# Kernel tuning notes

Hardware: AMD Instinct MI355X
Metric: run time of the kernel (lower is better)

The kernel has to match this reference:

```python
import jax, jax.numpy as jnp
import numpy as np

NUM_HEAD = 16
D = 1024
HEAD_DIM = D // NUM_HEAD
EPS = 1e-5


def setup_inputs() -> dict:
    key = jax.random.key(0)
    ks = jax.random.split(key, 7)
    B, S = 2, 2048
    s = 1.0 / np.sqrt(D)
    return {
        "x": jax.random.normal(ks[0], (B, S, D), dtype=jnp.float32),
        "wq": jax.random.uniform(ks[1], (D, D), jnp.float32, -s, s),
        "bq": jax.random.uniform(ks[2], (D,), jnp.float32, -s, s),
        "wk": jax.random.uniform(ks[3], (D, D), jnp.float32, -s, s),
        "bk": jax.random.uniform(ks[4], (D,), jnp.float32, -s, s),
        "wv": jax.random.uniform(ks[5], (D, D), jnp.float32, -s, s),
        "bv": jax.random.uniform(ks[6], (D,), jnp.float32, -s, s),
        "gamma": jnp.ones((D,), jnp.float32),
        "beta": jnp.zeros((D,), jnp.float32),
    }


def reference(x, wq, bq, wk, bk, wv, bv, gamma, beta):
    B, S, Dm = x.shape
    # Linear: x @ W^T + b (torch convention), then split heads -> [B, H, S, hd]
    def proj(w, b):
        y = jnp.einsum("bsd,ed->bse", x, w) + b
        return y.reshape(B, S, NUM_HEAD, HEAD_DIM).transpose(0, 2, 1, 3)

    q = proj(wq, bq)
    k = proj(wk, bk)
    v = proj(wv, bv)

    scores = jnp.einsum("bhqd,bhkd->bhqk", q, k) / np.sqrt(HEAD_DIM).astype(x.dtype)
    attn = jax.nn.softmax(scores, axis=-1)
    out = jnp.einsum("bhqk,bhkd->bhqd", attn, v)
    out = out.transpose(0, 2, 1, 3).reshape(B, S, Dm)

    out = out + x
    mu = jnp.mean(out, axis=-1, keepdims=True)
    var = jnp.var(out, axis=-1, keepdims=True)
    out = (out - mu) * jax.lax.rsqrt(var + EPS) * gamma + beta
    return out
```

## Files before the change

kernel.cpp:

```cpp
#include <hip/hip_runtime.h>

typedef unsigned short u16;
typedef unsigned int   u32;
typedef __bf16 bf16x8 __attribute__((ext_vector_type(8)));
typedef float  f32x4  __attribute__((ext_vector_type(4)));

#define D_MODEL 1024
#define SEQ     2048
#define NHEAD   16
#define HD      64
#define SOFTMAX_SCL 0.18033688011112042f

__device__ __forceinline__ u16 f2bf(float f) {
    u32 u;
    __builtin_memcpy(&u, &f, 4);
    u32 r = (u + 0x7fffu + ((u >> 16) & 1u)) >> 16;
    return (u16)r;
}
__device__ __forceinline__ float bf2f(u16 v) {
    u32 u = ((u32)v) << 16;
    float f;
    __builtin_memcpy(&f, &u, 4);
    return f;
}

__device__ __forceinline__ void async_copy16(const u16* g, u16* l) {
    __builtin_amdgcn_global_load_lds(
        (__attribute__((address_space(1))) void*)g,
        (__attribute__((address_space(3))) void*)l, 16, 0, 0);
}

__device__ __forceinline__ uint2 pack4(float a, float b, float c, float d) {
    uint2 r;
    r.x = (u32)f2bf(a) | ((u32)f2bf(b) << 16);
    r.y = (u32)f2bf(c) | ((u32)f2bf(d) << 16);
    return r;
}

#define NX4 ((2 * SEQ * D_MODEL) / 4)
#define NW4 ((D_MODEL * D_MODEL) / 4)
__global__ __launch_bounds__(256) void conv_all(
    const float* __restrict__ x,  const float* __restrict__ wq,
    const float* __restrict__ wk, const float* __restrict__ wv,
    u16* __restrict__ xb, u16* __restrict__ wqb,
    u16* __restrict__ wkb, u16* __restrict__ wvb)
{
    int i = blockIdx.x * 256 + threadIdx.x;
    const float* src; u16* dst; int off;
    if (i < NX4)            { src = x;  dst = xb;  off = i; }
    else if (i < NX4 + NW4) { src = wq; dst = wqb; off = i - NX4; }
    else if (i < NX4 + 2 * NW4) { src = wk; dst = wkb; off = i - NX4 - NW4; }
    else                    { src = wv; dst = wvb; off = i - NX4 - 2 * NW4; }
    float4 a = ((const float4*)src)[off];
    ushort4 o;
    o.x = f2bf(a.x); o.y = f2bf(a.y); o.z = f2bf(a.z); o.w = f2bf(a.w);
    ((ushort4*)dst)[off] = o;
}

__global__ __launch_bounds__(256) void qkv_gemm(
    const u16* __restrict__ xb,
    const u16* __restrict__ wqb, const float* __restrict__ bq,
    const u16* __restrict__ wkb, const float* __restrict__ bk,
    const u16* __restrict__ wvb, const float* __restrict__ bv,
    u16* __restrict__ qb, u16* __restrict__ kb, u16* __restrict__ vt)
{
    const int bid  = blockIdx.x;
    const int pair = bid % 24;
    const int by   = bid / 24;
    const int z    = pair >> 3;
    const int bx   = pair & 7;

    const u16* Ap; const u16* Bp;
    int m0, n0;
    if (z < 2) {
        Ap = (z == 1) ? wkb : wqb;  Bp = xb;
        m0 = bx * 128;
        n0 = by * 128;
    } else {
        Ap = xb;  Bp = wvb;
        m0 = by * 128;
        n0 = bx * 128;
    }

    __shared__ u16 As[128 * 64];
    __shared__ u16 Bs[128 * 64];

    const int tid  = threadIdx.x;
    const int wave = tid >> 6;
    const int lane = tid & 63;
    const int quad = lane >> 4;
    const int l16  = lane & 15;
    const int wm   = wave >> 1;
    const int wn   = wave & 1;
    const int swz  = l16 & 7;

    int rr[4], co[4];
#pragma unroll
    for (int t = 0; t < 4; ++t) {
        int ch = (wave * 4 + t) * 64 + lane;
        rr[t] = ch >> 3;
        co[t] = ((ch & 7) ^ (rr[t] & 7)) * 8;
    }

    f32x4 acc[4][4] = {};

    for (int kt = 0; kt < D_MODEL; kt += 64) {
        __syncthreads();
#pragma unroll
        for (int t = 0; t < 4; ++t) {
            int chbase = (wave * 4 + t) * 64;
            async_copy16(Ap + (size_t)(m0 + rr[t]) * D_MODEL + kt + co[t], As + chbase * 8);
            async_copy16(Bp + (size_t)(n0 + rr[t]) * D_MODEL + kt + co[t], Bs + chbase * 8);
        }
        __syncthreads();

#pragma unroll
        for (int kc = 0; kc < 2; ++kc) {
            bf16x8 af[4], bf_[4];
#pragma unroll
            for (int i = 0; i < 4; ++i)
                af[i] = *(const bf16x8*)&As[(wm * 64 + i * 16 + l16) * 64 + (((kc * 4 + quad) ^ swz) << 3)];
#pragma unroll
            for (int j = 0; j < 4; ++j)
                bf_[j] = *(const bf16x8*)&Bs[(wn * 64 + j * 16 + l16) * 64 + (((kc * 4 + quad) ^ swz) << 3)];
#pragma unroll
            for (int i = 0; i < 4; ++i)
#pragma unroll
                for (int j = 0; j < 4; ++j)
                    acc[i][j] = __builtin_amdgcn_mfma_f32_16x16x32_bf16(af[i], bf_[j], acc[i][j], 0, 0, 0);
        }
    }

    const int chunk_lo = (quad & 1) * 4;
    if (z < 2) {
        u16* out = (z == 1) ? kb : qb;
        const float* bi = (z == 1) ? bk : bq;
        const float scl = (z == 1) ? 1.0f : SOFTMAX_SCL;
        const int fblk = m0 + wm * 64;
#pragma unroll
        for (int i = 0; i < 4; ++i) {
            const int fb = fblk + i * 16 + quad * 4;
            float4 b4 = *(const float4*)&bi[fb];
            const int chunk = i * 2 + (quad >> 1);
#pragma unroll
            for (int j = 0; j < 4; ++j) {
                int token = n0 + wn * 64 + j * 16 + l16;
                uint2 pk = pack4((acc[i][j][0] + b4.x) * scl,
                                 (acc[i][j][1] + b4.y) * scl,
                                 (acc[i][j][2] + b4.z) * scl,
                                 (acc[i][j][3] + b4.w) * scl);
                size_t addr = (size_t)token * D_MODEL + fblk
                            + ((chunk ^ (token & 7)) << 3) + chunk_lo;
                *(uint2*)&out[addr] = pk;
            }
        }
    } else {
#pragma unroll
        for (int j = 0; j < 4; ++j) {
            int feat = n0 + wn * 64 + j * 16 + l16;
            float bias = bv[feat];
            int hh = feat >> 6, d = feat & 63;
            const size_t rowbase = ((size_t)hh * HD + d) * SEQ;
#pragma unroll
            for (int i = 0; i < 4; ++i) {
                int tok = m0 + wm * 64 + i * 16 + quad * 4;
                int b = tok >> 11, s = tok & 2047;
                const int chunk = i * 2 + (quad >> 1);
                uint2 pk = pack4(acc[i][j][0] + bias, acc[i][j][1] + bias,
                                 acc[i][j][2] + bias, acc[i][j][3] + bias);
                size_t addr = (size_t)b * NHEAD * HD * SEQ + rowbase
                            + (s & ~63) + ((chunk ^ (d & 7)) << 3) + chunk_lo;
                *(uint2*)&vt[addr] = pk;
            }
        }
    }
}

__global__ __launch_bounds__(256) void attn_kernel(
    const u16* __restrict__ qb, const u16* __restrict__ kb, const u16* __restrict__ vtg,
    u16* __restrict__ abp, float* __restrict__ lsums)
{
    const int bid  = blockIdx.x;
    const int bh   = bid & 31;
    const int b    = bh >> 4;
    const int h    = bh & 15;
    const int q0   = ((bid >> 5) & 15) * 128;
    const int half = bid >> 9;

    const int tid  = threadIdx.x;
    const int wave = tid >> 6;
    const int lane = tid & 63;
    const int quad = lane >> 4;
    const int l16  = lane & 15;
    const int swz  = l16 & 7;

    __shared__ u16 Ks[4096];
    __shared__ u16 Vt[4096];
    __shared__ u16 Ps[8 * 1024];

    const size_t kbase = (size_t)b * SEQ * D_MODEL + h * 64;
    const size_t vbase = (size_t)(b * NHEAD + h) * HD * SEQ;

    bf16x8 aq[2][2];
#pragma unroll
    for (int rb = 0; rb < 2; ++rb) {
        const int qrow = q0 + wave * 32 + rb * 16 + l16;
        const u16* qrp = qb + (size_t)qrow * D_MODEL + h * 64;
        aq[rb][0] = *(const bf16x8*)(qrp + ((quad ^ swz) << 3));
        aq[rb][1] = *(const bf16x8*)(qrp + (((4 + quad) ^ swz) << 3));
    }

    const int r0 = tid >> 3, r1 = (tid + 256) >> 3;
    const int cs8 = (tid & 7) * 8;
    const u16* kg0 = kb + kbase + (size_t)(half * 1024 + r0) * D_MODEL + cs8;
    const u16* kg1 = kb + kbase + (size_t)(half * 1024 + r1) * D_MODEL + cs8;
    const u16* vg0 = vtg + vbase + (size_t)r0 * SEQ + half * 1024 + cs8;
    const u16* vg1 = vtg + vbase + (size_t)r1 * SEQ + half * 1024 + cs8;
    const int wofs = wave * 512;

    f32x4 oacc[2][4] = {};
    float lsum[2][4] = {};

    for (int t = 0; t < 16; ++t) {
        __syncthreads();
        async_copy16(kg0, Ks + wofs);
        async_copy16(kg1, Ks + 2048 + wofs);
        async_copy16(vg0, Vt + wofs);
        async_copy16(vg1, Vt + 2048 + wofs);
        kg0 += 64 * D_MODEL; kg1 += 64 * D_MODEL;
        vg0 += 64;           vg1 += 64;
        __syncthreads();

        f32x4 sacc[2][4] = {};
#pragma unroll
        for (int c = 0; c < 2; ++c) {
            bf16x8 bk_[4];
#pragma unroll
            for (int nb = 0; nb < 4; ++nb)
                bk_[nb] = *(const bf16x8*)&Ks[(nb * 16 + l16) * 64 + (((c * 4 + quad) ^ swz) << 3)];
            __builtin_amdgcn_s_setprio(1);
#pragma unroll
            for (int rb = 0; rb < 2; ++rb)
#pragma unroll
                for (int nb = 0; nb < 4; ++nb)
                    sacc[rb][nb] = __builtin_amdgcn_mfma_f32_16x16x32_bf16(aq[rb][c], bk_[nb], sacc[rb][nb], 0, 0, 0);
            __builtin_amdgcn_s_setprio(0);
        }

#pragma unroll
        for (int rb = 0; rb < 2; ++rb)
#pragma unroll
            for (int r = 0; r < 4; ++r)
#pragma unroll
                for (int nb = 0; nb < 4; ++nb) {
                    float e = exp2f(sacc[rb][nb][r]);
                    lsum[rb][r] += e;
                    u32 bits;
                    __builtin_memcpy(&bits, &e, 4);
                    Ps[wave * 2048 + rb * 1024 + r * 256 + nb * 64 + lane] = (u16)(bits >> 16);
                }

#pragma unroll
        for (int c = 0; c < 2; ++c) {
            bf16x8 ap[2];
#pragma unroll
            for (int rb = 0; rb < 2; ++rb)
                ap[rb] = *(const bf16x8*)&Ps[wave * 2048 + rb * 1024 + (l16 & 3) * 256
                                             + (c * 2 + (quad >> 1)) * 64
                                             + (l16 >> 2) * 16 + (quad & 1) * 8];
            bf16x8 bv_[4];
#pragma unroll
            for (int nb = 0; nb < 4; ++nb)
                bv_[nb] = *(const bf16x8*)&Vt[(nb * 16 + l16) * 64 + (((c * 4 + quad) ^ swz) << 3)];
            __builtin_amdgcn_s_setprio(1);
#pragma unroll
            for (int rb = 0; rb < 2; ++rb)
#pragma unroll
                for (int nb = 0; nb < 4; ++nb)
                    oacc[rb][nb] = __builtin_amdgcn_mfma_f32_16x16x32_bf16(ap[rb], bv_[nb], oacc[rb][nb], 0, 0, 0);
            __builtin_amdgcn_s_setprio(0);
        }
    }

#pragma unroll
    for (int rb = 0; rb < 2; ++rb)
#pragma unroll
        for (int r = 0; r < 4; ++r) {
            float s = lsum[rb][r];
            s += __shfl_xor(s, 1, 64);
            s += __shfl_xor(s, 2, 64);
            s += __shfl_xor(s, 4, 64);
            s += __shfl_xor(s, 8, 64);
            int row = q0 + wave * 32 + rb * 16 + quad * 4 + r;
            if (l16 == 0)
                lsums[((size_t)bh * 2 + half) * SEQ + row] = s;
#pragma unroll
            for (int nb = 0; nb < 4; ++nb) {
                int d = nb * 16 + l16;
                abp[(size_t)half * SEQ * 2 * D_MODEL
                    + ((size_t)b * SEQ + row) * D_MODEL + h * 64 + d] = f2bf(oacc[rb][nb][r]);
            }
        }
}

__global__ __launch_bounds__(256) void add_ln(
    const u16* __restrict__ abp, const float* __restrict__ lsums,
    const float* __restrict__ x,
    const float* __restrict__ gamma, const float* __restrict__ beta,
    float* __restrict__ out)
{
    const int row = blockIdx.x;
    const int tid = threadIdx.x;
    const size_t rb = (size_t)row * D_MODEL;
    const int b = row >> 11, s = row & 2047;
    const int h = tid >> 4;
    const int bh = b * NHEAD + h;

    float l = lsums[(size_t)bh * 2 * SEQ + s] + lsums[((size_t)bh * 2 + 1) * SEQ + s];
    float inv = 1.0f / l;

    uint2 a0 = ((const uint2*)(abp + rb))[tid];
    uint2 a1 = ((const uint2*)(abp + (size_t)SEQ * 2 * D_MODEL + rb))[tid];
    float4 xb = ((const float4*)(x + rb))[tid];

    float v[4];
    v[0] = (bf2f((u16)(a0.x & 0xffff)) + bf2f((u16)(a1.x & 0xffff))) * inv + xb.x;
    v[1] = (bf2f((u16)(a0.x >> 16))    + bf2f((u16)(a1.x >> 16)))    * inv + xb.y;
    v[2] = (bf2f((u16)(a0.y & 0xffff)) + bf2f((u16)(a1.y & 0xffff))) * inv + xb.z;
    v[3] = (bf2f((u16)(a0.y >> 16))    + bf2f((u16)(a1.y >> 16)))    * inv + xb.w;

    float sm  = v[0] + v[1] + v[2] + v[3];
    float s2 = v[0]*v[0] + v[1]*v[1] + v[2]*v[2] + v[3]*v[3];
#pragma unroll
    for (int off = 1; off < 64; off <<= 1) {
        sm += __shfl_xor(sm, off, 64);
        s2 += __shfl_xor(s2, off, 64);
    }

    __shared__ float red[2][4];
    int wave = tid >> 6, lane = tid & 63;
    if (lane == 0) { red[0][wave] = sm; red[1][wave] = s2; }
    __syncthreads();
    float st  = red[0][0] + red[0][1] + red[0][2] + red[0][3];
    float s2t = red[1][0] + red[1][1] + red[1][2] + red[1][3];

    float mu   = st * (1.0f / D_MODEL);
    float var  = s2t * (1.0f / D_MODEL) - mu * mu;
    float rstd = rsqrtf(var + 1e-5f);

    float4 g  = ((const float4*)(gamma))[tid];
    float4 bt = ((const float4*)(beta))[tid];
    float4 o;
    o.x = (v[0] - mu) * rstd * g.x + bt.x;
    o.y = (v[1] - mu) * rstd * g.y + bt.y;
    o.z = (v[2] - mu) * rstd * g.z + bt.z;
    o.w = (v[3] - mu) * rstd * g.w + bt.w;
    ((float4*)(out + rb))[tid] = o;
}

extern "C" void kernel_launch(void* const* d_in, const int* in_sizes, int n_in,
                              void* d_out, int out_size, void* d_ws, size_t ws_size,
                              hipStream_t stream) {
    const float* x     = (const float*)d_in[0];
    const float* wq    = (const float*)d_in[1];
    const float* bq    = (const float*)d_in[2];
    const float* wk    = (const float*)d_in[3];
    const float* bk    = (const float*)d_in[4];
    const float* wv    = (const float*)d_in[5];
    const float* bv    = (const float*)d_in[6];
    const float* gamma = (const float*)d_in[7];
    const float* beta  = (const float*)d_in[8];
    float* outp = (float*)d_out;

    char* ws = (char*)d_ws;
    u16*   xb    = (u16*)(ws);
    u16*   wqb   = (u16*)(ws + ((size_t)8  << 20));
    u16*   wkb   = (u16*)(ws + ((size_t)10 << 20));
    u16*   wvb   = (u16*)(ws + ((size_t)12 << 20));
    u16*   qb    = (u16*)(ws + ((size_t)16 << 20));
    u16*   kb    = (u16*)(ws + ((size_t)24 << 20));
    u16*   vt    = (u16*)(ws + ((size_t)32 << 20));
    u16*   abp   = (u16*)(ws + ((size_t)40 << 20));
    float* lsums = (float*)(ws + ((size_t)56 << 20));

    conv_all<<<dim3((NX4 + 3 * NW4) / 256), 256, 0, stream>>>(
        x, wq, wk, wv, xb, wqb, wkb, wvb);
    qkv_gemm<<<dim3(24 * 32), 256, 0, stream>>>(xb, wqb, bq, wkb, bk, wvb, bv, qb, kb, vt);
    attn_kernel<<<dim3(1024), 256, 0, stream>>>(qb, kb, vt, abp, lsums);
    add_ln<<<dim3(2 * SEQ), 256, 0, stream>>>(abp, lsums, x, gamma, beta, outp);
}
```

Measured before the change: 203.3 us.

## Double-buffer K/V tiles in attention kernel with async prefetch

Doubles the K and V shared-memory buffers so the next tile's async global-to-LDS copy is issued before computing on the current tile, waiting with a partial vmcnt instead of a full barrier-copy-barrier. It halves the per-wave P staging buffer by reusing one 1024-element region per row block, reading it back immediately after writing. It also adds a launch-bounds occupancy hint of four blocks. Together these aim to hide global load latency behind MFMA work and keep LDS usage flat. The risk is added register pressure from the occupancy hint, and correctness now depends on the hand-written waitcnt counts.

Result: slower. 214.6 us (+5.6%).

```diff
diff --git a/kernel.cpp b/kernel.cpp
--- a/kernel.cpp
+++ b/kernel.cpp
@@ -176,7 +176,7 @@
     }
 }
 
-__global__ __launch_bounds__(256) void attn_kernel(
+__global__ __launch_bounds__(256, 4) void attn_kernel(
     const u16* __restrict__ qb, const u16* __restrict__ kb, const u16* __restrict__ vtg,
     u16* __restrict__ abp, float* __restrict__ lsums)
 {
@@ -194,9 +194,9 @@
     const int l16  = lane & 15;
     const int swz  = l16 & 7;
 
-    __shared__ u16 Ks[4096];
-    __shared__ u16 Vt[4096];
-    __shared__ u16 Ps[8 * 1024];
+    __shared__ u16 Ks[2 * 4096];
+    __shared__ u16 Vt[2 * 4096];
+    __shared__ u16 Ps[4 * 1024];
 
     const size_t kbase = (size_t)b * SEQ * D_MODEL + h * 64;
     const size_t vbase = (size_t)(b * NHEAD + h) * HD * SEQ;
@@ -221,15 +221,35 @@
     f32x4 oacc[2][4] = {};
     float lsum[2][4] = {};
 
+    async_copy16(kg0, Ks + wofs);
+    async_copy16(kg1, Ks + 2048 + wofs);
+    async_copy16(vg0, Vt + wofs);
+    async_copy16(vg1, Vt + 2048 + wofs);
+    kg0 += 64 * D_MODEL; kg1 += 64 * D_MODEL;
+    vg0 += 64;           vg1 += 64;
+
+    u16* Psw = Ps + wave * 1024;
+
     for (int t = 0; t < 16; ++t) {
-        __syncthreads();
-        async_copy16(kg0, Ks + wofs);
-        async_copy16(kg1, Ks + 2048 + wofs);
-        async_copy16(vg0, Vt + wofs);
-        async_copy16(vg1, Vt + 2048 + wofs);
-        kg0 += 64 * D_MODEL; kg1 += 64 * D_MODEL;
-        vg0 += 64;           vg1 += 64;
-        __syncthreads();
+        const int cur = (t & 1) << 12;
+        const int nxt = cur ^ 4096;
+
+        __builtin_amdgcn_s_barrier();
+        if (t < 15) {
+            async_copy16(kg0, Ks + nxt + wofs);
+            async_copy16(kg1, Ks + nxt + 2048 + wofs);
+            async_copy16(vg0, Vt + nxt + wofs);
+            async_copy16(vg1, Vt + nxt + 2048 + wofs);
+            kg0 += 64 * D_MODEL; kg1 += 64 * D_MODEL;
+            vg0 += 64;           vg1 += 64;
+            asm volatile("s_waitcnt vmcnt(4)" ::: "memory");
+        } else {
+            asm volatile("s_waitcnt vmcnt(0)" ::: "memory");
+        }
+        __builtin_amdgcn_s_barrier();
+
+        const u16* Kc = Ks + cur;
+        const u16* Vc = Vt + cur;
 
         f32x4 sacc[2][4] = {};
 #pragma unroll
@@ -237,7 +257,7 @@
             bf16x8 bk_[4];
 #pragma unroll
             for (int nb = 0; nb < 4; ++nb)
-                bk_[nb] = *(const bf16x8*)&Ks[(nb * 16 + l16) * 64 + (((c * 4 + quad) ^ swz) << 3)];
+                bk_[nb] = *(const bf16x8*)&Kc[(nb * 16 + l16) * 64 + (((c * 4 + quad) ^ swz) << 3)];
             __builtin_amdgcn_s_setprio(1);
 #pragma unroll
             for (int rb = 0; rb < 2; ++rb)
@@ -247,8 +267,9 @@
             __builtin_amdgcn_s_setprio(0);
         }
 
-#pragma unroll
-        for (int rb = 0; rb < 2; ++rb)
+        bf16x8 ap[2][2];
+#pragma unroll
+        for (int rb = 0; rb < 2; ++rb) {
 #pragma unroll
             for (int r = 0; r < 4; ++r)
 #pragma unroll
@@ -257,27 +278,27 @@
                     lsum[rb][r] += e;
                     u32 bits;
                     __builtin_memcpy(&bits, &e, 4);
-                    Ps[wave * 2048 + rb * 1024 + r * 256 + nb * 64 + lane] = (u16)(bits >> 16);
+                    Psw[r * 256 + nb * 64 + lane] = (u16)(bits >> 16);
                 }
+#pragma unroll
+            for (int c = 0; c < 2; ++c)
+                ap[rb][c] = *(const bf16x8*)&Psw[(l16 & 3) * 256
+                                                 + (c * 2 + (quad >> 1)) * 64
+                                                 + (l16 >> 2) * 16 + (quad & 1) * 8];
+        }
 
 #pragma unroll
         for (int c = 0; c < 2; ++c) {
-            bf16x8 ap[2];
+            bf16x8 bv_[4];
+#pragma unroll
+            for (int nb = 0; nb < 4; ++nb)
+                bv_[nb] = *(const bf16x8*)&Vc[(nb * 16 + l16) * 64 + (((c * 4 + quad) ^ swz) << 3)];
+            __builtin_amdgcn_s_setprio(1);
 #pragma unroll
             for (int rb = 0; rb < 2; ++rb)
-                ap[rb] = *(const bf16x8*)&Ps[wave * 2048 + rb * 1024 + (l16 & 3) * 256
-                                             + (c * 2 + (quad >> 1)) * 64
-                                             + (l16 >> 2) * 16 + (quad & 1) * 8];
-            bf16x8 bv_[4];
-#pragma unroll
-            for (int nb = 0; nb < 4; ++nb)
-                bv_[nb] = *(const bf16x8*)&Vt[(nb * 16 + l16) * 64 + (((c * 4 + quad) ^ swz) << 3)];
-            __builtin_amdgcn_s_setprio(1);
-#pragma unroll
-            for (int rb = 0; rb < 2; ++rb)
 #pragma unroll
                 for (int nb = 0; nb < 4; ++nb)
-                    oacc[rb][nb] = __builtin_amdgcn_mfma_f32_16x16x32_bf16(ap[rb], bv_[nb], oacc[rb][nb], 0, 0, 0);
+                    oacc[rb][nb] = __builtin_amdgcn_mfma_f32_16x16x32_bf16(ap[rb][c], bv_[nb], oacc[rb][nb], 0, 0, 0);
             __builtin_amdgcn_s_setprio(0);
         }
     }
```
